# Kernel tuning notes

Hardware: AMD Instinct MI355X
Metric: run time of the kernel (lower is better)

## Reference

```python
import jax, jax.numpy as jnp
from jax import lax
import numpy as np

B, N, F_IN = 8, 8192, 64
NPOINT, K = 2048, 16
C0 = F_IN + 3  # use_xyz concat
EPS = 1e-5


def setup_inputs() -> dict:
    key = jax.random.key(0)
    ks = jax.random.split(key, 8)
    xyz = jax.random.normal(ks[0], (B, 3, N), dtype=jnp.float32)
    points = jax.random.normal(ks[1], (B, F_IN, N), dtype=jnp.float32)
    def conv_params(k, cout, cin):
        W = jax.random.normal(k, (cout, cin), dtype=jnp.float32) * (1.0 / np.sqrt(cin))
        return W, jnp.zeros((cout,), jnp.float32)
    W1, b1 = conv_params(ks[2], 64, C0)
    W2, b2 = conv_params(ks[3], 64, 64)
    W3, b3 = conv_params(ks[4], 128, 64)
    g1 = jnp.ones((64,), jnp.float32); be1 = jnp.zeros((64,), jnp.float32)
    g2 = jnp.ones((64,), jnp.float32); be2 = jnp.zeros((64,), jnp.float32)
    return dict(xyz=xyz, points=points, W1=W1, b1=b1, g1=g1, be1=be1,
                W2=W2, b2=b2, g2=g2, be2=be2, W3=W3, b3=b3)


def _fps(xyz_bn3, npoint):
    # furthest point sampling; starts at index 0 (as PointNet++ CUDA op)
    b, n, _ = xyz_bn3.shape
    init_idx = jnp.zeros((b,), jnp.int32)
    dist0 = jnp.full((b, n), 1e10, xyz_bn3.dtype)

    def body(carry, _):
        dist, last = carry
        p = jnp.take_along_axis(xyz_bn3, last[:, None, None], axis=1)  # (b,1,3)
        d = jnp.sum((xyz_bn3 - p) ** 2, axis=-1)                       # (b,n)
        dist = jnp.minimum(dist, d)
        nxt = jnp.argmax(dist, axis=-1).astype(jnp.int32)
        return (dist, nxt), nxt

    (_, _), rest = lax.scan(body, (dist0, init_idx), None, length=npoint - 1)
    return jnp.concatenate([init_idx[None], rest], axis=0).T  # (b, npoint)


def _gather_feat(feat, idx):
    # feat: (B,C,N), idx: (B,...) -> (B,C,...)
    return jax.vmap(lambda f, i: f[:, i])(feat, idx)


def _conv_bn_relu(x, W, b, g, be):
    # 1x1 Conv2d + BatchNorm2d(training batch stats) + ReLU
    y = jnp.einsum('oi,bipk->bopk', W, x) + b[None, :, None, None]
    mean = y.mean(axis=(0, 2, 3))
    var = y.var(axis=(0, 2, 3))
    y = (y - mean[None, :, None, None]) * lax.rsqrt(var + EPS)[None, :, None, None]
    y = y * g[None, :, None, None] + be[None, :, None, None]
    return jax.nn.relu(y)


def reference(xyz, points, W1, b1, g1, be1, W2, b2, g2, be2, W3, b3):
    # --- sample_and_group_knn ---
    xyz_t = jnp.transpose(xyz, (0, 2, 1))             # (B,N,3)
    fps_idx = _fps(xyz_t, NPOINT)                      # (B,npoint)
    new_xyz = _gather_feat(xyz, fps_idx)               # (B,3,npoint)
    q = jnp.transpose(new_xyz, (0, 2, 1))              # (B,npoint,3)
    # squared distances (B,npoint,N)
    sq = (jnp.sum(q ** 2, -1)[:, :, None]
          + jnp.sum(xyz_t ** 2, -1)[:, None, :]
          - 2.0 * jnp.einsum('bqc,bnc->bqn', q, xyz_t))
    _, idx = lax.top_k(-sq, K)                         # (B,npoint,K) nearest
    grouped_xyz = _gather_feat(xyz, idx)               # (B,3,npoint,K)
    grouped_xyz = grouped_xyz - new_xyz[:, :, :, None]
    grouped_pts = _gather_feat(points, idx)            # (B,f,npoint,K)
    new_points = jnp.concatenate([grouped_xyz, grouped_pts], axis=1)  # (B,67,npoint,K)
    # --- shared MLP (1x1 convs) + max-pool over neighbors ---
    h = _conv_bn_relu(new_points, W1, b1, g1, be1)
    h = _conv_bn_relu(h, W2, b2, g2, be2)
    h = jnp.einsum('oi,bipk->bopk', W3, h) + b3[None, :, None, None]  # no bn/act
    new_feat = jnp.max(h, axis=3)                      # (B,128,npoint)
    return new_xyz, new_feat
```

## Files before the change

### kernel.cpp

```cpp
#include <hip/hip_runtime.h>
#pragma clang fp contract(off)

#define BB 8
#define NN 8192
#define NP 2048
#define KNbr 16
#define FIN 64
#define NPOS (BB*NP*KNbr)
#define NCONS 248
#define AG __HIP_MEMORY_SCOPE_AGENT

typedef float f32x2 __attribute__((ext_vector_type(2)));
typedef unsigned long long u64;

__device__ __forceinline__ float sq3(float x, float y, float z) {
  return __fadd_rn(__fadd_rn(__fmul_rn(x,x), __fmul_rn(y,y)), __fmul_rn(z,z));
}

__device__ __forceinline__ int wave_imax(int x) {
  x = max(x, __builtin_amdgcn_update_dpp(0, x, 0x111, 0xf, 0xf, false));
  x = max(x, __builtin_amdgcn_update_dpp(0, x, 0x112, 0xf, 0xf, false));
  x = max(x, __builtin_amdgcn_update_dpp(0, x, 0x114, 0xf, 0xf, false));
  x = max(x, __builtin_amdgcn_update_dpp(0, x, 0x118, 0xf, 0xf, false));
  x = max(x, __builtin_amdgcn_update_dpp(0, x, 0x142, 0xa, 0xf, false));
  x = max(x, __builtin_amdgcn_update_dpp(0, x, 0x143, 0xc, 0xf, false));
  return __builtin_amdgcn_readlane(x, 63);
}
__device__ __forceinline__ unsigned wave_umin(unsigned x) {
  x = min(x, (unsigned)__builtin_amdgcn_update_dpp(-1, (int)x, 0x111, 0xf, 0xf, false));
  x = min(x, (unsigned)__builtin_amdgcn_update_dpp(-1, (int)x, 0x112, 0xf, 0xf, false));
  x = min(x, (unsigned)__builtin_amdgcn_update_dpp(-1, (int)x, 0x114, 0xf, 0xf, false));
  x = min(x, (unsigned)__builtin_amdgcn_update_dpp(-1, (int)x, 0x118, 0xf, 0xf, false));
  x = min(x, (unsigned)__builtin_amdgcn_update_dpp(-1, (int)x, 0x142, 0xa, 0xf, false));
  x = min(x, (unsigned)__builtin_amdgcn_update_dpp(-1, (int)x, 0x143, 0xc, 0xf, false));
  return (unsigned)__builtin_amdgcn_readlane((int)x, 63);
}

__global__ __launch_bounds__(256,1) void k_front2(const float* __restrict__ xyz,
                                                  const float* __restrict__ pts,
                                                  const float* __restrict__ W1,
                                                  const float* __restrict__ b1,
                                                  float4* __restrict__ xyzw,
                                                  float* __restrict__ qwf,
                                                  float* __restrict__ pre,
                                                  float* __restrict__ stats,
                                                  int* __restrict__ prog,
                                                  int* __restrict__ pflag,
                                                  float* __restrict__ ybuf,
                                                  float* __restrict__ newxyz) {
  __shared__ float tx[NN], ty[NN], tz[NN];
  __shared__ float4 res[NP];
  __shared__ u64 skey[2][4];
  int blk = blockIdx.x, tid = threadIdx.x;
  int lane = tid & 63, wave = tid >> 6;

  if (blk >= 8) {
    for (int g = (blk-8)*256 + tid; g < BB*NN; g += NCONS*256) {
      int b = g >> 13, n = g & (NN-1);
      const float* p = xyz + (size_t)b*3*NN;
      float x = p[n], y = p[NN+n], z = p[2*NN+n];
      xyzw[g] = make_float4(x, y, z, sq3(x,y,z));
      const float* P = pts + (size_t)b*FIN*NN + n;
      float pv[64];
      #pragma unroll
      for (int i=0;i<64;++i) pv[i] = P[(size_t)i*NN];
      float4* outp = (float4*)(pre + (size_t)g*64);
      for (int og=0; og<16; ++og) {
        float acc[4];
        #pragma unroll
        for (int oo=0;oo<4;++oo) {
          int o = og*4+oo;
          float s = b1[o];
          #pragma unroll
          for (int i=0;i<64;++i) s = fmaf(W1[o*67+3+i], pv[i], s);
          acc[oo] = s;
        }
        outp[og] = make_float4(acc[0],acc[1],acc[2],acc[3]);
      }
    }
    if (blk == 8) stats[tid] = 0.f;
    __syncthreads();
    if (tid == 0) {
      __threadfence();
      __hip_atomic_store(&pflag[blk-8], 1, __ATOMIC_RELEASE, AG);
    }
    bool ok = false;
    while (!ok) {
      int v = 1;
      for (int i = lane; i < NCONS; i += 64)
        v &= (__hip_atomic_load(&pflag[i], __ATOMIC_RELAXED, AG) == 1);
      ok = (bool)__all(v);
      if (!ok) __builtin_amdgcn_s_sleep(32);
    }
    __threadfence();

    int slot = (blk-8)*4 + wave;
    float W1a = W1[lane*67+0], W1b = W1[lane*67+1], W1c = W1[lane*67+2];
    float sum = 0.f, ss = 0.f;
    for (int qi = slot; qi < BB*NP; qi += NCONS*4) {
      int t = qi >> 3, b = qi & 7;
      while (__hip_atomic_load(&prog[b*32], __ATOMIC_RELAXED, AG) <= t)
        __builtin_amdgcn_s_sleep(16);
      const float* qp = qwf + ((size_t)(b*NP + t))*4;
      float qx  = __hip_atomic_load(qp+0, __ATOMIC_RELAXED, AG);
      float qy  = __hip_atomic_load(qp+1, __ATOMIC_RELAXED, AG);
      float qz  = __hip_atomic_load(qp+2, __ATOMIC_RELAXED, AG);
      float qw4 = __hip_atomic_load(qp+3, __ATOMIC_RELAXED, AG);
      const float4* base = xyzw + (size_t)b*NN;
      float ld = 3.0e38f; int li = 0x7fffffff;
      float taud = 3.0e38f; int taui = 0x7fffffff;
      for (int c = 0; c < 128; ++c) {
        int idx = c*64 + lane;
        float4 P = base[idx];
        float dot = __fadd_rn(__fadd_rn(__fmul_rn(P.x,qx), __fmul_rn(P.y,qy)), __fmul_rn(P.z,qz));
        float dd  = __fsub_rn(__fadd_rn(qw4, P.w), __fmul_rn(2.0f, dot));
        bool better = (dd < taud) || (dd == taud && idx < taui);
        u64 mask = __ballot(better);
        while (mask) {
          int src = __ffsll(mask) - 1;
          mask &= mask - 1;
          float bd = __shfl(dd, src, 64);
          int   bi = __shfl(idx, src, 64);
          bool before = (ld < bd) || (ld == bd && li < bi);
          float sd = __shfl_up(ld, 1, 64);
          int   si = __shfl_up(li, 1, 64);
          int   bp = __shfl_up((int)before, 1, 64);
          bool take_new = !before && (lane == 0 || bp);
          float nd = before ? ld : (take_new ? bd : sd);
          int   ni = before ? li : (take_new ? bi : si);
          if (lane < 16) { ld = nd; li = ni; }
          taud = __shfl(ld, 15, 64);
          taui = __shfl(li, 15, 64);
        }
      }
      const float* preb = pre + (size_t)b*NN*64;
      float* yb = ybuf + ((size_t)(b*NP + t))*16*64;
      for (int l=0;l<16;++l) {
        int n = __shfl(li, l, 64);
        float4 P = base[n];
        float dx=__fsub_rn(P.x,qx), dy=__fsub_rn(P.y,qy), dz=__fsub_rn(P.z,qz);
        float v = fmaf(W1a, dx, fmaf(W1b, dy, fmaf(W1c, dz, preb[(size_t)n*64 + lane])));
        yb[l*64 + lane] = v;
        sum += v; ss = fmaf(v, v, ss);
      }
    }
    atomicAdd(&stats[lane], sum);
    atomicAdd(&stats[64+lane], ss);
    return;
  }

  int b = blk;
  const float* pxyz = xyz + (size_t)b*3*NN;
  f32x2 px[16], py[16], pz[16], d2[16];
  #pragma unroll
  for (int j=0;j<16;++j) {
    int i = j*512 + 2*tid;
    float2 xv = *(const float2*)(pxyz + i);
    float2 yv = *(const float2*)(pxyz + NN + i);
    float2 zv = *(const float2*)(pxyz + 2*NN + i);
    tx[i] = xv.x; tx[i+1] = xv.y;
    ty[i] = yv.x; ty[i+1] = yv.y;
    tz[i] = zv.x; tz[i+1] = zv.y;
    px[j] = f32x2{xv.x, xv.y};
    py[j] = f32x2{yv.x, yv.y};
    pz[j] = f32x2{zv.x, zv.y};
    d2[j] = f32x2{1e10f, 1e10f};
  }
  float cx = pxyz[0], cy = pxyz[NN], cz = pxyz[2*NN];
  if (tid==0) {
    res[0] = make_float4(cx, cy, cz, 0.f);
    __hip_atomic_store(qwf + (size_t)(b*NP)*4 + 0, cx, __ATOMIC_RELAXED, AG);
    __hip_atomic_store(qwf + (size_t)(b*NP)*4 + 1, cy, __ATOMIC_RELAXED, AG);
    __hip_atomic_store(qwf + (size_t)(b*NP)*4 + 2, cz, __ATOMIC_RELAXED, AG);
    __hip_atomic_store(qwf + (size_t)(b*NP)*4 + 3, sq3(cx,cy,cz), __ATOMIC_RELAXED, AG);
    __hip_atomic_store(&prog[b*32], 1, __ATOMIC_RELEASE, AG);
  }
  int w = tid>>6;
  __syncthreads();
  for (int t=1;t<NP;++t) {
    f32x2 cx2 = {cx,cx}, cy2 = {cy,cy}, cz2 = {cz,cz};
    #pragma unroll
    for (int j=0;j<16;++j) {
      f32x2 dx = px[j]-cx2, dy = py[j]-cy2, dz = pz[j]-cz2;
      f32x2 dd = (dx*dx + dy*dy) + dz*dz;
#if __has_builtin(__builtin_elementwise_min)
      d2[j] = __builtin_elementwise_min(d2[j], dd);
#else
      d2[j].x = fminf(d2[j].x, dd.x);
      d2[j].y = fminf(d2[j].y, dd.y);
#endif
    }
    float tv[16]; int tk[16];
    #pragma unroll
    for (int j=0;j<16;++j) {
      bool r = d2[j].y > d2[j].x;
      tv[j] = r ? d2[j].y : d2[j].x;
      tk[j] = r ? 2*j+1 : 2*j;
    }
    #pragma unroll
    for (int j=0;j<8;++j) { bool r = tv[j+8] > tv[j]; if (r){tv[j]=tv[j+8]; tk[j]=tk[j+8];} }
    #pragma unroll
    for (int j=0;j<4;++j) { bool r = tv[j+4] > tv[j]; if (r){tv[j]=tv[j+4]; tk[j]=tk[j+4];} }
    #pragma unroll
    for (int j=0;j<2;++j) { bool r = tv[j+2] > tv[j]; if (r){tv[j]=tv[j+2]; tk[j]=tk[j+2];} }
    bool rr = tv[1] > tv[0];
    float lmax = rr ? tv[1] : tv[0];
    int   k    = rr ? tk[1] : tk[0];
    unsigned gidx = (unsigned)((k>>1)*512 + 2*tid + (k&1));
    int mb = wave_imax(__float_as_int(lmax));
    unsigned cand = (__float_as_int(lmax) == mb) ? gidx : 0xFFFFFFFFu;
    unsigned wwin = wave_umin(cand);
    int buf = t & 1;
    if ((tid & 63) == 0)
      skey[buf][w] = ((u64)(unsigned)mb << 32) | (u64)(0xFFFFFFFFu - wwin);
    __syncthreads();
    if ((t & 63) == 0) {
      int e = t - 64 + (tid >> 2), comp = tid & 3;
      float4 r = res[e];
      float v = (comp==0) ? r.x : (comp==1) ? r.y : (comp==2) ? r.z : sq3(r.x,r.y,r.z);
      __hip_atomic_store(qwf + ((size_t)(b*NP + e))*4 + comp, v, __ATOMIC_RELAXED, AG);
    } else if ((t & 63) == 1 && t > 64 && tid == 0) {
      __hip_atomic_store(&prog[b*32], t-1, __ATOMIC_RELEASE, AG);
    }
    u64 mk = skey[buf][0];
    if (skey[buf][1] > mk) mk = skey[buf][1];
    if (skey[buf][2] > mk) mk = skey[buf][2];
    if (skey[buf][3] > mk) mk = skey[buf][3];
    unsigned widx = 0xFFFFFFFFu - (unsigned)(mk & 0xFFFFFFFFull);
    cx = tx[widx]; cy = ty[widx]; cz = tz[widx];
    if (tid == (t & 255))
      res[t] = make_float4(cx, cy, cz, 0.f);
  }
  __syncthreads();
  float* outx = newxyz + (size_t)b*3*NP;
  #pragma unroll
  for (int s=0;s<8;++s) {
    int i = s*256 + tid;
    float4 r = res[i];
    *(float4*)(qwf + ((size_t)(b*NP + i))*4) = make_float4(r.x, r.y, r.z, sq3(r.x,r.y,r.z));
    outx[i] = r.x; outx[NP + i] = r.y; outx[2*NP + i] = r.z;
  }
  __syncthreads();
  if (tid == 0) {
    __threadfence();
    __hip_atomic_store(&prog[b*32], NP, __ATOMIC_RELEASE, AG);
  }
}

__global__ __launch_bounds__(256) void k_act(float* __restrict__ y,
                                             const float* __restrict__ st,
                                             const float* __restrict__ gam,
                                             const float* __restrict__ bet) {
  __shared__ __align__(16) float sS[64], sT[64];
  int tid = threadIdx.x;
  if (tid < 64) {
    float mean = st[tid] * (1.0f/NPOS);
    float var  = st[64+tid] * (1.0f/NPOS) - mean*mean;
    float istd = 1.0f / sqrtf(var + 1e-5f);
    float s = gam[tid]*istd;
    sS[tid] = s;
    sT[tid] = bet[tid] - mean*s;
  }
  __syncthreads();
  size_t g = (size_t)blockIdx.x*256 + tid;
  float4* Y = (float4*)y;
  #pragma unroll
  for (int r=0;r<4;++r) {
    size_t f4 = g + (size_t)r*1048576;
    int c0 = (int)((f4*4) & 63);
    float4 s4 = *(const float4*)(sS + c0);
    float4 t4 = *(const float4*)(sT + c0);
    float4 v = Y[f4];
    v.x = fmaxf(0.f, fmaf(v.x, s4.x, t4.x));
    v.y = fmaxf(0.f, fmaf(v.y, s4.y, t4.y));
    v.z = fmaxf(0.f, fmaf(v.z, s4.z, t4.z));
    v.w = fmaxf(0.f, fmaf(v.w, s4.w, t4.w));
    Y[f4] = v;
  }
}

__device__ __forceinline__ float dot64(const float4* x, const float* W, float init) {
  float a0 = init, a1 = 0.f, a2 = 0.f, a3 = 0.f;
  #pragma unroll
  for (int j=0;j<16;++j) {
    float4 v = x[j];
    a0 = fmaf(v.x, W[4*j],   a0);
    a1 = fmaf(v.y, W[4*j+1], a1);
    a2 = fmaf(v.z, W[4*j+2], a2);
    a3 = fmaf(v.w, W[4*j+3], a3);
  }
  return (a0+a1)+(a2+a3);
}

__global__ __launch_bounds__(256) void k_conv2v(float* __restrict__ y,
                                                const float* __restrict__ W2,
                                                const float* __restrict__ b2,
                                                float* __restrict__ st2) {
  __shared__ float r1[4][64], r2[4][64];
  int wave = threadIdx.x>>6;
  int wid = blockIdx.x*4 + wave;
  int lane = threadIdx.x & 63;
  float W[64];
  #pragma unroll
  for (int j=0;j<16;++j) {
    float4 t = *(const float4*)(W2 + (size_t)lane*64 + j*4);
    W[4*j]=t.x; W[4*j+1]=t.y; W[4*j+2]=t.z; W[4*j+3]=t.w;
  }
  float bb = b2[lane];
  size_t p0 = (size_t)wid*128;
  const float4* src = (const float4*)(y + p0*64);
  float4 xa[16], xb[16];
  float sum = 0.f, ss = 0.f;
  #pragma unroll
  for (int j=0;j<16;++j) xa[j] = src[j];
  for (int p=0;p<128;p+=2) {
    #pragma unroll
    for (int j=0;j<16;++j) xb[j] = src[(p+1)*16 + j];
    float acc = dot64(xa, W, bb);
    y[(p0+p)*64 + lane] = acc;
    sum += acc; ss = fmaf(acc, acc, ss);
    if (p+2 < 128) {
      #pragma unroll
      for (int j=0;j<16;++j) xa[j] = src[(p+2)*16 + j];
    }
    float acc2 = dot64(xb, W, bb);
    y[(p0+p+1)*64 + lane] = acc2;
    sum += acc2; ss = fmaf(acc2, acc2, ss);
  }
  r1[wave][lane] = sum; r2[wave][lane] = ss;
  __syncthreads();
  if (threadIdx.x < 64) {
    int l = threadIdx.x;
    float t1 = r1[0][l]+r1[1][l]+r1[2][l]+r1[3][l];
    float t2 = r2[0][l]+r2[1][l]+r2[2][l]+r2[3][l];
    atomicAdd(&st2[l], t1);
    atomicAdd(&st2[64+l], t2);
  }
}

__global__ __launch_bounds__(256) void k_c3v(const float* __restrict__ y,
                                             const float* __restrict__ W3,
                                             const float* __restrict__ b3,
                                             float* __restrict__ feat) {
  int wid = blockIdx.x*4 + (threadIdx.x>>6);
  int lane = threadIdx.x & 63;
  int h = wid & 1, chunk = wid >> 1;
  float W[64];
  #pragma unroll
  for (int j=0;j<16;++j) {
    float4 t = *(const float4*)(W3 + ((size_t)(h*64+lane))*64 + j*4);
    W[4*j]=t.x; W[4*j+1]=t.y; W[4*j+2]=t.z; W[4*j+3]=t.w;
  }
  float bb = b3[h*64+lane];
  const float4* src = (const float4*)(y + (size_t)chunk*16*16*64);
  float4 xa[16], xb[16];
  #pragma unroll
  for (int j=0;j<16;++j) xa[j] = src[j];
  int pos = 0;
  for (int q=0;q<16;++q) {
    float m = -3.0e38f;
    #pragma unroll 1
    for (int k=0;k<16;k+=2) {
      #pragma unroll
      for (int j=0;j<16;++j) xb[j] = src[(pos+1)*16 + j];
      m = fmaxf(m, dot64(xa, W, bb));
      if (pos+2 < 256) {
        #pragma unroll
        for (int j=0;j<16;++j) xa[j] = src[(pos+2)*16 + j];
      }
      m = fmaxf(m, dot64(xb, W, bb));
      pos += 2;
    }
    int gq = chunk*16 + q;
    int b = gq >> 11, qq = gq & (NP-1);
    feat[((size_t)(b*128 + h*64 + lane))*NP + qq] = m;
  }
}

extern "C" void kernel_launch(void* const* d_in, const int* in_sizes, int n_in,
                              void* d_out, int out_size, void* d_ws, size_t ws_size,
                              hipStream_t stream) {
  const float* xyz = (const float*)d_in[0];
  const float* pts = (const float*)d_in[1];
  const float* W1  = (const float*)d_in[2];
  const float* b1  = (const float*)d_in[3];
  const float* g1  = (const float*)d_in[4];
  const float* be1 = (const float*)d_in[5];
  const float* W2  = (const float*)d_in[6];
  const float* b2  = (const float*)d_in[7];
  const float* g2  = (const float*)d_in[8];
  const float* be2 = (const float*)d_in[9];
  const float* W3  = (const float*)d_in[10];
  const float* b3  = (const float*)d_in[11];
  float* out = (float*)d_out;
  float* ws  = (float*)d_ws;

  float4* xyzw  = (float4*)ws;
  float*  qwf   = ws + 262144;
  float*  pre   = ws + 1654784;
  float*  ybuf  = ws + 5849088;
  float*  stats = ws + 22626304;
  int*    prog  = (int*)(ws + 22626560);
  int*    pflag = (int*)(ws + 22626816);

  k_front2<<<256, 256, 0, stream>>>(xyz, pts, W1, b1, xyzw, qwf, pre, stats,
                                    prog, pflag, ybuf, out);
  k_act   <<<4096, 256, 0, stream>>>(ybuf, stats, g1, be1);
  k_conv2v<<<512, 256, 0, stream>>>(ybuf, W2, b2, stats + 128);
  k_act   <<<4096, 256, 0, stream>>>(ybuf, stats + 128, g2, be2);
  k_c3v   <<<512, 256, 0, stream>>>(ybuf, W3, b3, out + 49152);
}
```

Measured before the change: 2.510 ms.

## Fuse BatchNorm+ReLU into the conv2 and conv3 kernels via LDS staging

Removes the two standalone k_act passes. The folded scale and shift are now computed inside k_conv2f and k_c3f. Each block loads a 64-position activation tile, normalizes and ReLUs it into shared memory, then computes the 1x1 conv from LDS with many more, smaller blocks. This drops two full read-write sweeps over the large intermediate buffer and two launches, at the cost of extra LDS use and a different work split that may lower per-wave reuse.

```diff
diff --git a/kernel.cpp b/kernel.cpp
--- a/kernel.cpp
+++ b/kernel.cpp
@@ -247,38 +247,6 @@
   }
 }
 
-__global__ __launch_bounds__(256) void k_act(float* __restrict__ y,
-                                             const float* __restrict__ st,
-                                             const float* __restrict__ gam,
-                                             const float* __restrict__ bet) {
-  __shared__ __align__(16) float sS[64], sT[64];
-  int tid = threadIdx.x;
-  if (tid < 64) {
-    float mean = st[tid] * (1.0f/NPOS);
-    float var  = st[64+tid] * (1.0f/NPOS) - mean*mean;
-    float istd = 1.0f / sqrtf(var + 1e-5f);
-    float s = gam[tid]*istd;
-    sS[tid] = s;
-    sT[tid] = bet[tid] - mean*s;
-  }
-  __syncthreads();
-  size_t g = (size_t)blockIdx.x*256 + tid;
-  float4* Y = (float4*)y;
-  #pragma unroll
-  for (int r=0;r<4;++r) {
-    size_t f4 = g + (size_t)r*1048576;
-    int c0 = (int)((f4*4) & 63);
-    float4 s4 = *(const float4*)(sS + c0);
-    float4 t4 = *(const float4*)(sT + c0);
-    float4 v = Y[f4];
-    v.x = fmaxf(0.f, fmaf(v.x, s4.x, t4.x));
-    v.y = fmaxf(0.f, fmaf(v.y, s4.y, t4.y));
-    v.z = fmaxf(0.f, fmaf(v.z, s4.z, t4.z));
-    v.w = fmaxf(0.f, fmaf(v.w, s4.w, t4.w));
-    Y[f4] = v;
-  }
-}
-
 __device__ __forceinline__ float dot64(const float4* x, const float* W, float init) {
   float a0 = init, a1 = 0.f, a2 = 0.f, a3 = 0.f;
   #pragma unroll
@@ -292,14 +260,25 @@
   return (a0+a1)+(a2+a3);
 }
 
-__global__ __launch_bounds__(256) void k_conv2v(float* __restrict__ y,
+__global__ __launch_bounds__(256) void k_conv2f(float* __restrict__ y,
                                                 const float* __restrict__ W2,
                                                 const float* __restrict__ b2,
+                                                const float* __restrict__ st1,
+                                                const float* __restrict__ g1,
+                                                const float* __restrict__ be1,
                                                 float* __restrict__ st2) {
+  __shared__ __align__(16) float4 xs[1024];
+  __shared__ __align__(16) float sS[64], sT[64];
   __shared__ float r1[4][64], r2[4][64];
-  int wave = threadIdx.x>>6;
-  int wid = blockIdx.x*4 + wave;
-  int lane = threadIdx.x & 63;
+  int tid = threadIdx.x, lane = tid & 63, wave = tid >> 6;
+  if (tid < 64) {
+    float mean = st1[tid] * (1.0f/NPOS);
+    float var  = st1[64+tid] * (1.0f/NPOS) - mean*mean;
+    float istd = 1.0f / sqrtf(var + 1e-5f);
+    float s = g1[tid]*istd;
+    sS[tid] = s;
+    sT[tid] = be1[tid] - mean*s;
+  }
   float W[64];
   #pragma unroll
   for (int j=0;j<16;++j) {
@@ -307,74 +286,101 @@
     W[4*j]=t.x; W[4*j+1]=t.y; W[4*j+2]=t.z; W[4*j+3]=t.w;
   }
   float bb = b2[lane];
-  size_t p0 = (size_t)wid*128;
-  const float4* src = (const float4*)(y + p0*64);
-  float4 xa[16], xb[16];
+  __syncthreads();
+  size_t tbase = (size_t)blockIdx.x * 1024;
+  float4* Y4 = (float4*)y;
+  #pragma unroll
+  for (int i=0;i<4;++i) {
+    int idx = i*256 + tid;
+    float4 v = Y4[tbase + idx];
+    int c0 = (idx & 15)*4;
+    float4 s4 = *(const float4*)(sS + c0);
+    float4 t4 = *(const float4*)(sT + c0);
+    v.x = fmaxf(0.f, fmaf(v.x, s4.x, t4.x));
+    v.y = fmaxf(0.f, fmaf(v.y, s4.y, t4.y));
+    v.z = fmaxf(0.f, fmaf(v.z, s4.z, t4.z));
+    v.w = fmaxf(0.f, fmaf(v.w, s4.w, t4.w));
+    xs[idx] = v;
+  }
+  __syncthreads();
   float sum = 0.f, ss = 0.f;
-  #pragma unroll
-  for (int j=0;j<16;++j) xa[j] = src[j];
-  for (int p=0;p<128;p+=2) {
-    #pragma unroll
-    for (int j=0;j<16;++j) xb[j] = src[(p+1)*16 + j];
-    float acc = dot64(xa, W, bb);
-    y[(p0+p)*64 + lane] = acc;
+  size_t pos0 = (size_t)blockIdx.x*64 + wave*16;
+  #pragma unroll 1
+  for (int p=0;p<16;++p) {
+    float acc = dot64(&xs[(wave*16+p)*16], W, bb);
+    y[(pos0+p)*64 + lane] = acc;
     sum += acc; ss = fmaf(acc, acc, ss);
-    if (p+2 < 128) {
-      #pragma unroll
-      for (int j=0;j<16;++j) xa[j] = src[(p+2)*16 + j];
-    }
-    float acc2 = dot64(xb, W, bb);
-    y[(p0+p+1)*64 + lane] = acc2;
-    sum += acc2; ss = fmaf(acc2, acc2, ss);
   }
   r1[wave][lane] = sum; r2[wave][lane] = ss;
   __syncthreads();
-  if (threadIdx.x < 64) {
-    int l = threadIdx.x;
-    float t1 = r1[0][l]+r1[1][l]+r1[2][l]+r1[3][l];
-    float t2 = r2[0][l]+r2[1][l]+r2[2][l]+r2[3][l];
-    atomicAdd(&st2[l], t1);
-    atomicAdd(&st2[64+l], t2);
-  }
-}
-
-__global__ __launch_bounds__(256) void k_c3v(const float* __restrict__ y,
+  if (tid < 64) {
+    float t1 = r1[0][tid]+r1[1][tid]+r1[2][tid]+r1[3][tid];
+    float t2 = r2[0][tid]+r2[1][tid]+r2[2][tid]+r2[3][tid];
+    atomicAdd(&st2[tid], t1);
+    atomicAdd(&st2[64+tid], t2);
+  }
+}
+
+__global__ __launch_bounds__(256) void k_c3f(const float* __restrict__ y,
                                              const float* __restrict__ W3,
                                              const float* __restrict__ b3,
+                                             const float* __restrict__ st2,
+                                             const float* __restrict__ g2,
+                                             const float* __restrict__ be2,
                                              float* __restrict__ feat) {
-  int wid = blockIdx.x*4 + (threadIdx.x>>6);
-  int lane = threadIdx.x & 63;
-  int h = wid & 1, chunk = wid >> 1;
+  __shared__ __align__(16) float4 xs[1024];
+  __shared__ __align__(16) float sS[64], sT[64];
+  int tid = threadIdx.x, lane = tid & 63, wave = tid >> 6;
+  int h = wave & 1, qpair = wave >> 1;
+  if (tid < 64) {
+    float mean = st2[tid] * (1.0f/NPOS);
+    float var  = st2[64+tid] * (1.0f/NPOS) - mean*mean;
+    float istd = 1.0f / sqrtf(var + 1e-5f);
+    float s = g2[tid]*istd;
+    sS[tid] = s;
+    sT[tid] = be2[tid] - mean*s;
+  }
+  int O = h*64 + lane;
   float W[64];
   #pragma unroll
   for (int j=0;j<16;++j) {
-    float4 t = *(const float4*)(W3 + ((size_t)(h*64+lane))*64 + j*4);
+    float4 t = *(const float4*)(W3 + (size_t)O*64 + j*4);
     W[4*j]=t.x; W[4*j+1]=t.y; W[4*j+2]=t.z; W[4*j+3]=t.w;
   }
-  float bb = b3[h*64+lane];
-  const float4* src = (const float4*)(y + (size_t)chunk*16*16*64);
-  float4 xa[16], xb[16];
-  #pragma unroll
-  for (int j=0;j<16;++j) xa[j] = src[j];
-  int pos = 0;
-  for (int q=0;q<16;++q) {
+  float bb = b3[O];
+  __syncthreads();
+  size_t tbase = (size_t)blockIdx.x * 1024;
+  const float4* Y4 = (const float4*)y;
+  #pragma unroll
+  for (int i=0;i<4;++i) {
+    int idx = i*256 + tid;
+    float4 v = Y4[tbase + idx];
+    int c0 = (idx & 15)*4;
+    float4 s4 = *(const float4*)(sS + c0);
+    float4 t4 = *(const float4*)(sT + c0);
+    v.x = fmaxf(0.f, fmaf(v.x, s4.x, t4.x));
+    v.y = fmaxf(0.f, fmaf(v.y, s4.y, t4.y));
+    v.z = fmaxf(0.f, fmaf(v.z, s4.z, t4.z));
+    v.w = fmaxf(0.f, fmaf(v.w, s4.w, t4.w));
+    xs[idx] = v;
+  }
+  __syncthreads();
+  float mq[2];
+  #pragma unroll 1
+  for (int q=0;q<2;++q) {
     float m = -3.0e38f;
     #pragma unroll 1
-    for (int k=0;k<16;k+=2) {
-      #pragma unroll
-      for (int j=0;j<16;++j) xb[j] = src[(pos+1)*16 + j];
-      m = fmaxf(m, dot64(xa, W, bb));
-      if (pos+2 < 256) {
-        #pragma unroll
-        for (int j=0;j<16;++j) xa[j] = src[(pos+2)*16 + j];
-      }
-      m = fmaxf(m, dot64(xb, W, bb));
-      pos += 2;
-    }
-    int gq = chunk*16 + q;
-    int b = gq >> 11, qq = gq & (NP-1);
-    feat[((size_t)(b*128 + h*64 + lane))*NP + qq] = m;
-  }
+    for (int k=0;k<16;++k) {
+      int p = (qpair*2 + q)*16 + k;
+      m = fmaxf(m, dot64(&xs[p*16], W, bb));
+    }
+    mq[q] = m;
+  }
+  int gq0 = blockIdx.x*4 + qpair*2;
+  int b = gq0 >> 11, qq = gq0 & (NP-1);
+  float* fp = feat + ((size_t)(b*128 + O))*NP + qq;
+  fp[0] = mq[0];
+  fp[1] = mq[1];
 }
 
 extern "C" void kernel_launch(void* const* d_in, const int* in_sizes, int n_in,
@@ -405,8 +411,6 @@
 
   k_front2<<<256, 256, 0, stream>>>(xyz, pts, W1, b1, xyzw, qwf, pre, stats,
                                     prog, pflag, ybuf, out);
-  k_act   <<<4096, 256, 0, stream>>>(ybuf, stats, g1, be1);
-  k_conv2v<<<512, 256, 0, stream>>>(ybuf, W2, b2, stats + 128);
-  k_act   <<<4096, 256, 0, stream>>>(ybuf, stats + 128, g2, be2);
-  k_c3v   <<<512, 256, 0, stream>>>(ybuf, W3, b3, out + 49152);
-}
+  k_conv2f<<<4096, 256, 0, stream>>>(ybuf, W2, b2, stats, g1, be1, stats + 128);
+  k_c3f   <<<4096, 256, 0, stream>>>(ybuf, W3, b3, stats + 128, g2, be2, out + 49152);
+}
```

Result: faster. 2.333 ms (-7.1%).
